# Kernel tuning notes

Measured on AMD Instinct MI355X. Metric: run time of the kernel, lower is better.

## Reference

```python
import jax, jax.numpy as jnp
import numpy as np

B, S, H, E, K = 4, 2048, 2048, 8, 2


def setup_inputs() -> dict:
    key = jax.random.key(0)
    k1, k2, k3 = jax.random.split(key, 3)
    scale = 1.0 / np.sqrt(H)
    return {
        "x": jax.random.normal(k1, (B, S, H), dtype=jnp.float32),
        "Wg": jax.random.normal(k2, (H, E), dtype=jnp.float32) * scale,
        "bg": jnp.zeros((E,), dtype=jnp.float32),
        "W": jax.random.normal(k3, (E, H, H), dtype=jnp.float32) * scale,
        "b": jnp.zeros((E, H), dtype=jnp.float32),
        "topk": K,
    }


def reference(x, Wg, bg, W, b, topk):
    Bsz, Sl, Hd = x.shape
    n_exp = W.shape[0]
    hs = x.reshape(-1, Hd)                              # [T, H] flattened tokens
    # Router: linear gate -> softmax -> top-k -> renormalize
    router_logits = hs @ Wg + bg                        # [T, E]
    probs = jax.nn.softmax(router_logits, axis=-1)
    top_w, sel = jax.lax.top_k(probs, topk)             # [T, K]
    top_w = top_w / jnp.sum(top_w, axis=-1, keepdims=True)
    # Per-token combine coefficient for each expert (sums weights over top-k slots)
    coef = jnp.einsum("tk,tke->te", top_w,
                      jax.nn.one_hot(sel, n_exp, dtype=hs.dtype))  # [T, E]
    # Dense grouped expert MLP: y_e = hs @ W_e + b_e, then weighted combine.
    h = jnp.einsum("th,ehf->etf", hs, W) + b[:, None, :]  # [E, T, H]
    out = jnp.einsum("te,etf->tf", coef, h)               # [T, H]
    return out.reshape(Bsz, Sl, Hd), router_logits
```

## Files before the change

### kernel.cpp

```cpp
#include <hip/hip_runtime.h>
#include <math.h>

#define T_TOK 8192
#define HD    2048
#define NE    8
#define BM    128
#define BN    128
#define NT    (HD / 64)
#define MAXT  136
#define RMAX  17408

typedef __bf16 bf16x4 __attribute__((ext_vector_type(4)));
typedef __bf16 bf16x8 __attribute__((ext_vector_type(8)));
typedef float  f32x4  __attribute__((ext_vector_type(4)));

#define GLOAD16(src, dst)                                                              \
    __builtin_amdgcn_global_load_lds((__attribute__((address_space(1))) void*)(src),   \
                                     (__attribute__((address_space(3))) void*)(dst),   \
                                     16, 0, 0)

__global__ __launch_bounds__(256) void router_cvt_kernel(
    const float* __restrict__ x, const float* __restrict__ Wg,
    const float* __restrict__ bg, float* __restrict__ logits_out,
    int* __restrict__ tok_exp, float* __restrict__ tok_w,
    __bf16* __restrict__ xb)
{
    const int lane = threadIdx.x & 63;
    const int wv   = threadIdx.x >> 6;
    const int t    = blockIdx.x * 4 + wv;
    const float* xr  = x  + (size_t)t * HD;
    __bf16*      xbr = xb + (size_t)t * HD;

    float acc[8] = {0.f,0.f,0.f,0.f,0.f,0.f,0.f,0.f};
#pragma unroll
    for (int j = 0; j < 8; ++j) {
        const int h0 = j * 256 + lane * 4;
        float4 xv = *reinterpret_cast<const float4*>(xr + h0);
        bf16x4 bv;
        bv[0] = (__bf16)xv.x; bv[1] = (__bf16)xv.y;
        bv[2] = (__bf16)xv.z; bv[3] = (__bf16)xv.w;
        *reinterpret_cast<bf16x4*>(xbr + h0) = bv;

        const float4* wg = reinterpret_cast<const float4*>(Wg + (size_t)h0 * NE);
        float xs[4] = {xv.x, xv.y, xv.z, xv.w};
#pragma unroll
        for (int r = 0; r < 4; ++r) {
            float4 wa = wg[r * 2], wb = wg[r * 2 + 1];
            acc[0] += xs[r] * wa.x; acc[1] += xs[r] * wa.y;
            acc[2] += xs[r] * wa.z; acc[3] += xs[r] * wa.w;
            acc[4] += xs[r] * wb.x; acc[5] += xs[r] * wb.y;
            acc[6] += xs[r] * wb.z; acc[7] += xs[r] * wb.w;
        }
    }
#pragma unroll
    for (int off = 32; off; off >>= 1) {
#pragma unroll
        for (int e = 0; e < 8; ++e) acc[e] += __shfl_xor(acc[e], off);
    }
    if (lane == 0) {
        float lg[8];
#pragma unroll
        for (int e = 0; e < 8; ++e) lg[e] = acc[e] + bg[e];
        float4* lo = reinterpret_cast<float4*>(logits_out + (size_t)t * NE);
        lo[0] = make_float4(lg[0], lg[1], lg[2], lg[3]);
        lo[1] = make_float4(lg[4], lg[5], lg[6], lg[7]);
        int i0 = 0;
        for (int e = 1; e < 8; ++e) if (lg[e] > lg[i0]) i0 = e;
        int i1 = (i0 == 0) ? 1 : 0;
        for (int e = 0; e < 8; ++e) if (e != i0 && lg[e] > lg[i1]) i1 = e;
        float d = expf(lg[i1] - lg[i0]);
        float inv = 1.0f / (1.0f + d);
        tok_exp[t * 2]     = i0;
        tok_exp[t * 2 + 1] = i1;
        tok_w[t * 2]       = inv;
        tok_w[t * 2 + 1]   = d * inv;
    }
}

__global__ __launch_bounds__(256) void hist_kernel(const int* __restrict__ tok_exp,
                                                   int* __restrict__ cnt)
{
    __shared__ int h[NE];
    if (threadIdx.x < NE) h[threadIdx.x] = 0;
    __syncthreads();
    int s = blockIdx.x * 256 + threadIdx.x;
    atomicAdd(&h[tok_exp[s]], 1);
    __syncthreads();
    if (threadIdx.x < NE) atomicAdd(&cnt[threadIdx.x], h[threadIdx.x]);
}

__global__ __launch_bounds__(256) void wt_kernel(const float* __restrict__ W,
                                                 __bf16* __restrict__ Wt)
{
    const int e  = blockIdx.z;
    const int k0 = blockIdx.y * 64;
    const int f0 = blockIdx.x * 64;
    __shared__ float T[64][65];

    const int t  = threadIdx.x;
    const int fi = (t & 15) * 4;
    const int kb = t >> 4;
    const float* src = W + (size_t)e * HD * HD + (size_t)(k0 + kb) * HD + f0 + fi;
#pragma unroll
    for (int j = 0; j < 4; ++j) {
        float4 v = *reinterpret_cast<const float4*>(src + (size_t)j * 16 * HD);
        int k = kb + j * 16;
        T[k][fi + 0] = v.x;
        T[k][fi + 1] = v.y;
        T[k][fi + 2] = v.z;
        T[k][fi + 3] = v.w;
    }
    __syncthreads();
    const int f  = t >> 2;
    const int kc = (t & 3) * 16;
    bf16x8 o0, o1;
#pragma unroll
    for (int j = 0; j < 8; ++j) o0[j] = (__bf16)T[kc + j][f];
#pragma unroll
    for (int j = 0; j < 8; ++j) o1[j] = (__bf16)T[kc + 8 + j][f];
    __bf16* dst = Wt + (size_t)e * HD * HD + (size_t)(f0 + f) * HD + k0 + kc;
    *reinterpret_cast<bf16x8*>(dst)     = o0;
    *reinterpret_cast<bf16x8*>(dst + 8) = o1;
}

__global__ void scan_kernel(const int* __restrict__ cnt, int* __restrict__ cursor,
                            int* __restrict__ tile_exp, int* __restrict__ tile_row0,
                            int* __restrict__ ntiles)
{
    if (threadIdx.x == 0) {
        int off = 0, nt = 0;
        for (int e = 0; e < NE; ++e) {
            cursor[e] = off;
            int c = cnt[e];
            int tiles = (c + 127) >> 7;
            for (int i = 0; i < tiles; ++i) {
                tile_exp[nt]  = e;
                tile_row0[nt] = off + (i << 7);
                ++nt;
            }
            off += tiles << 7;
        }
        *ntiles = nt;
    }
}

__global__ __launch_bounds__(256) void scatter_kernel(
    const int* __restrict__ tok_exp, const float* __restrict__ tok_w,
    int* __restrict__ cursor, int* __restrict__ row_token, float* __restrict__ row_coef)
{
    __shared__ int lcnt[NE];
    __shared__ int lbase[NE];
    const int tid = threadIdx.x;
    if (tid < NE) lcnt[tid] = 0;
    __syncthreads();
    const int s = blockIdx.x * 256 + tid;
    const int e = tok_exp[s];
    const int r = atomicAdd(&lcnt[e], 1);
    __syncthreads();
    if (tid < NE) lbase[tid] = atomicAdd(&cursor[tid], lcnt[tid]);
    __syncthreads();
    const int pos = lbase[e] + r;
    row_token[pos] = s >> 1;
    row_coef[pos]  = tok_w[s];
}

__global__ __launch_bounds__(256, 2) void moe_gemm_128(
    const __bf16* __restrict__ xb, const __bf16* __restrict__ Wt,
    const float* __restrict__ bexp,
    const int* __restrict__ tile_exp, const int* __restrict__ tile_row0,
    const int* __restrict__ ntiles_p, const int* __restrict__ row_token,
    const float* __restrict__ row_coef, float* __restrict__ out)
{
    const int rt = blockIdx.y;
    if (rt >= *ntiles_p) return;
    const int e  = tile_exp[rt];
    const int r0 = tile_row0[rt];
    const int cb = blockIdx.x * BN;

    __shared__ __align__(16) char lds[65536];

    const int tid  = threadIdx.x;
    const int lane = tid & 63;
    const int wv   = tid >> 6;
    const int wr   = (wv >> 1) * 64;
    const int wc   = (wv & 1) * 64;

    const int colS = ((((tid & 7) * 16) ^ (((tid >> 3) & 7) << 4))) >> 1;

    const __bf16* srcA[4];
    const __bf16* srcB[4];
#pragma unroll
    for (int i = 0; i < 4; ++i) {
        int gr  = i * 32 + (tid >> 3);
        int tok = row_token[r0 + gr];
        if (tok < 0) tok = 0;
        srcA[i] = xb + (size_t)tok * HD + colS;
        srcB[i] = Wt + ((size_t)e << 22) + (size_t)(cb + gr) * HD + colS;
    }

    f32x4 acc[4][4];
#pragma unroll
    for (int m = 0; m < 4; ++m)
#pragma unroll
        for (int n = 0; n < 4; ++n) acc[m][n] = (f32x4){0.f, 0.f, 0.f, 0.f};

    const int fr    = lane & 15;
    const int swz   = (lane & 7) << 4;
    const int koff0 = (((lane >> 4) * 16)      ) ^ swz;
    const int koff1 = (((lane >> 4) * 16) + 64 ) ^ swz;

    {
        char* d0 = lds + wv * 1024;
        char* d1 = d0 + 32768;
#pragma unroll
        for (int i = 0; i < 4; ++i) GLOAD16(srcA[i], d0 + i * 4096);
#pragma unroll
        for (int i = 0; i < 4; ++i) GLOAD16(srcB[i], d0 + 16384 + i * 4096);
#pragma unroll
        for (int i = 0; i < 4; ++i) GLOAD16(srcA[i] + 64, d1 + i * 4096);
#pragma unroll
        for (int i = 0; i < 4; ++i) GLOAD16(srcB[i] + 64, d1 + 16384 + i * 4096);
    }

#pragma unroll 2
    for (int t = 0; t < NT; ++t) {
        if (t < NT - 1) { asm volatile("s_waitcnt vmcnt(8)" ::: "memory"); }
        else            { asm volatile("s_waitcnt vmcnt(0)" ::: "memory"); }
        __builtin_amdgcn_s_barrier();

        const char* ab = lds + (t & 1) * 32768;
        const char* bb = ab + 16384;

        bf16x8 bfr0[4], bfr1[4];
#pragma unroll
        for (int n = 0; n < 4; ++n) {
            int rowb = (wc + n * 16 + fr) << 7;
            bfr0[n] = *reinterpret_cast<const bf16x8*>(bb + (rowb + koff0));
            bfr1[n] = *reinterpret_cast<const bf16x8*>(bb + (rowb + koff1));
        }
        __builtin_amdgcn_s_setprio(1);
#pragma unroll
        for (int m = 0; m < 4; ++m) {
            int rowa = (wr + m * 16 + fr) << 7;
            bf16x8 a0 = *reinterpret_cast<const bf16x8*>(ab + (rowa + koff0));
            bf16x8 a1 = *reinterpret_cast<const bf16x8*>(ab + (rowa + koff1));
#pragma unroll
            for (int n = 0; n < 4; ++n) {
                acc[m][n] = __builtin_amdgcn_mfma_f32_16x16x32_bf16(a0, bfr0[n], acc[m][n], 0, 0, 0);
                acc[m][n] = __builtin_amdgcn_mfma_f32_16x16x32_bf16(a1, bfr1[n], acc[m][n], 0, 0, 0);
            }
        }
        __builtin_amdgcn_s_setprio(0);

        if (t < NT - 2) {
            asm volatile("s_waitcnt lgkmcnt(0)" ::: "memory");
            __builtin_amdgcn_s_barrier();
            const int nk = (t + 2) * 64;
            char* dA = lds + (t & 1) * 32768 + wv * 1024;
#pragma unroll
            for (int i = 0; i < 4; ++i) GLOAD16(srcA[i] + nk, dA + i * 4096);
#pragma unroll
            for (int i = 0; i < 4; ++i) GLOAD16(srcB[i] + nk, dA + 16384 + i * 4096);
        }
    }

    const int rj = (lane >> 4) * 4;
    float bias_[4];
#pragma unroll
    for (int n = 0; n < 4; ++n)
        bias_[n] = bexp[(size_t)e * HD + cb + wc + n * 16 + fr];

#pragma unroll
    for (int m = 0; m < 4; ++m) {
        const int lr = wr + m * 16 + rj;
        int tok[4]; float cf[4];
#pragma unroll
        for (int j = 0; j < 4; ++j) {
            tok[j] = row_token[r0 + lr + j];
            cf[j]  = row_coef[r0 + lr + j];
        }
#pragma unroll
        for (int n = 0; n < 4; ++n) {
            const int f = cb + wc + n * 16 + fr;
#pragma unroll
            for (int j = 0; j < 4; ++j) {
                if (tok[j] >= 0)
                    atomicAdd(&out[(size_t)tok[j] * HD + f], (acc[m][n][j] + bias_[n]) * cf[j]);
            }
        }
    }
}

extern "C" void kernel_launch(void* const* d_in, const int* in_sizes, int n_in,
                              void* d_out, int out_size, void* d_ws, size_t ws_size,
                              hipStream_t stream)
{
    (void)in_sizes; (void)n_in; (void)out_size; (void)ws_size;

    const float* x  = (const float*)d_in[0];
    const float* Wg = (const float*)d_in[1];
    const float* bg = (const float*)d_in[2];
    const float* W  = (const float*)d_in[3];
    const float* b  = (const float*)d_in[4];

    float* out    = (float*)d_out;
    float* logits = out + (size_t)T_TOK * HD;

    char* p = (char*)d_ws;
    int*   cnt       = (int*)p;   p += NE * 4;
    int*   cursor    = (int*)p;   p += NE * 4;
    int*   ntiles    = (int*)p;   p += 8;
    int*   tile_exp  = (int*)p;   p += MAXT * 4;
    int*   tile_row0 = (int*)p;   p += MAXT * 4;
    int*   tok_exp   = (int*)p;   p += T_TOK * 2 * 4;
    float* tok_w     = (float*)p; p += T_TOK * 2 * 4;
    int*   row_token = (int*)p;   p += RMAX * 4;
    float* row_coef  = (float*)p; p += RMAX * 4;
    p = (char*)(((size_t)p + 255) & ~(size_t)255);
    __bf16* xb = (__bf16*)p;      p += (size_t)T_TOK * HD * 2;
    __bf16* Wt = (__bf16*)p;      p += (size_t)NE * HD * HD * 2;

    hipMemsetAsync(cnt, 0, NE * 4, stream);
    hipMemsetAsync(row_token, 0xFF, RMAX * 4, stream);
    hipMemsetAsync(out, 0, (size_t)T_TOK * HD * sizeof(float), stream);

    router_cvt_kernel<<<T_TOK / 4, 256, 0, stream>>>(x, Wg, bg, logits,
                                                     tok_exp, tok_w, xb);
    wt_kernel<<<dim3(HD / 64, HD / 64, NE), 256, 0, stream>>>(W, Wt);
    hist_kernel<<<T_TOK * 2 / 256, 256, 0, stream>>>(tok_exp, cnt);
    scan_kernel<<<1, 64, 0, stream>>>(cnt, cursor, tile_exp, tile_row0, ntiles);
    scatter_kernel<<<T_TOK * 2 / 256, 256, 0, stream>>>(tok_exp, tok_w, cursor,
                                                        row_token, row_coef);

    dim3 grid(HD / BN, MAXT);
    moe_gemm_128<<<grid, 256, 0, stream>>>(xb, Wt, b, tile_exp, tile_row0, ntiles,
                                           row_token, row_coef, out);
}
```

Measured before the change: 334.0 us.

## Load expert weight fragments straight into registers instead of staging through LDS

The B operand (expert weights) is now fetched from global memory directly into a double-buffered register array in MFMA fragment layout, instead of going through LDS with global_load_lds. Only the A tile is staged in LDS, so the LDS footprint halves and the launch bound is raised to 3 blocks per CU to use the freed space. The goal is to cut LDS traffic and ds_read latency and to raise occupancy. The cost is about 64 extra VGPRs for the fragments, which risks spills under the tighter register cap. B reads become less coalesced and are duplicated across waves that share columns, and compiler-inserted waits on the register loads may break the hand-tuned vmcnt pipelining.

```diff
diff --git a/kernel.cpp b/kernel.cpp
--- a/kernel.cpp
+++ b/kernel.cpp
@@ -18,6 +18,8 @@
     __builtin_amdgcn_global_load_lds((__attribute__((address_space(1))) void*)(src),   \
                                      (__attribute__((address_space(3))) void*)(dst),   \
                                      16, 0, 0)
+
+#define MEMFENCE() asm volatile("" ::: "memory")
 
 __global__ __launch_bounds__(256) void router_cvt_kernel(
     const float* __restrict__ x, const float* __restrict__ Wg,
@@ -164,7 +166,7 @@
     row_coef[pos]  = tok_w[s];
 }
 
-__global__ __launch_bounds__(256, 2) void moe_gemm_128(
+__global__ __launch_bounds__(256, 3) void moe_gemm_128(
     const __bf16* __restrict__ xb, const __bf16* __restrict__ Wt,
     const float* __restrict__ bexp,
     const int* __restrict__ tile_exp, const int* __restrict__ tile_row0,
@@ -177,7 +179,7 @@
     const int r0 = tile_row0[rt];
     const int cb = blockIdx.x * BN;
 
-    __shared__ __align__(16) char lds[65536];
+    __shared__ __align__(16) char lds[32768];
 
     const int tid  = threadIdx.x;
     const int lane = tid & 63;
@@ -188,15 +190,17 @@
     const int colS = ((((tid & 7) * 16) ^ (((tid >> 3) & 7) << 4))) >> 1;
 
     const __bf16* srcA[4];
-    const __bf16* srcB[4];
 #pragma unroll
     for (int i = 0; i < 4; ++i) {
         int gr  = i * 32 + (tid >> 3);
         int tok = row_token[r0 + gr];
         if (tok < 0) tok = 0;
         srcA[i] = xb + (size_t)tok * HD + colS;
-        srcB[i] = Wt + ((size_t)e << 22) + (size_t)(cb + gr) * HD + colS;
-    }
+    }
+
+    const int fr = lane & 15;
+    const int fk = (lane >> 4) * 8;
+    const __bf16* bbase = Wt + ((size_t)e << 22) + (size_t)(cb + wc + fr) * HD + fk;
 
     f32x4 acc[4][4];
 #pragma unroll
@@ -204,40 +208,41 @@
 #pragma unroll
         for (int n = 0; n < 4; ++n) acc[m][n] = (f32x4){0.f, 0.f, 0.f, 0.f};
 
-    const int fr    = lane & 15;
     const int swz   = (lane & 7) << 4;
     const int koff0 = (((lane >> 4) * 16)      ) ^ swz;
     const int koff1 = (((lane >> 4) * 16) + 64 ) ^ swz;
 
+    bf16x8 breg[2][4][2];
+
     {
         char* d0 = lds + wv * 1024;
-        char* d1 = d0 + 32768;
+        char* d1 = d0 + 16384;
 #pragma unroll
         for (int i = 0; i < 4; ++i) GLOAD16(srcA[i], d0 + i * 4096);
 #pragma unroll
-        for (int i = 0; i < 4; ++i) GLOAD16(srcB[i], d0 + 16384 + i * 4096);
+        for (int n = 0; n < 4; ++n)
+#pragma unroll
+            for (int ks = 0; ks < 2; ++ks)
+                breg[0][n][ks] = *reinterpret_cast<const bf16x8*>(bbase + n * 16 * HD + ks * 32);
+        MEMFENCE();
 #pragma unroll
         for (int i = 0; i < 4; ++i) GLOAD16(srcA[i] + 64, d1 + i * 4096);
 #pragma unroll
-        for (int i = 0; i < 4; ++i) GLOAD16(srcB[i] + 64, d1 + 16384 + i * 4096);
+        for (int n = 0; n < 4; ++n)
+#pragma unroll
+            for (int ks = 0; ks < 2; ++ks)
+                breg[1][n][ks] = *reinterpret_cast<const bf16x8*>(bbase + n * 16 * HD + 64 + ks * 32);
+        MEMFENCE();
     }
 
 #pragma unroll 2
     for (int t = 0; t < NT; ++t) {
-        if (t < NT - 1) { asm volatile("s_waitcnt vmcnt(8)" ::: "memory"); }
+        if (t < NT - 1) { asm volatile("s_waitcnt vmcnt(12)" ::: "memory"); }
         else            { asm volatile("s_waitcnt vmcnt(0)" ::: "memory"); }
         __builtin_amdgcn_s_barrier();
 
-        const char* ab = lds + (t & 1) * 32768;
-        const char* bb = ab + 16384;
-
-        bf16x8 bfr0[4], bfr1[4];
-#pragma unroll
-        for (int n = 0; n < 4; ++n) {
-            int rowb = (wc + n * 16 + fr) << 7;
-            bfr0[n] = *reinterpret_cast<const bf16x8*>(bb + (rowb + koff0));
-            bfr1[n] = *reinterpret_cast<const bf16x8*>(bb + (rowb + koff1));
-        }
+        const char* ab = lds + (t & 1) * 16384;
+
         __builtin_amdgcn_s_setprio(1);
 #pragma unroll
         for (int m = 0; m < 4; ++m) {
@@ -246,8 +251,8 @@
             bf16x8 a1 = *reinterpret_cast<const bf16x8*>(ab + (rowa + koff1));
 #pragma unroll
             for (int n = 0; n < 4; ++n) {
-                acc[m][n] = __builtin_amdgcn_mfma_f32_16x16x32_bf16(a0, bfr0[n], acc[m][n], 0, 0, 0);
-                acc[m][n] = __builtin_amdgcn_mfma_f32_16x16x32_bf16(a1, bfr1[n], acc[m][n], 0, 0, 0);
+                acc[m][n] = __builtin_amdgcn_mfma_f32_16x16x32_bf16(a0, breg[t & 1][n][0], acc[m][n], 0, 0, 0);
+                acc[m][n] = __builtin_amdgcn_mfma_f32_16x16x32_bf16(a1, breg[t & 1][n][1], acc[m][n], 0, 0, 0);
             }
         }
         __builtin_amdgcn_s_setprio(0);
@@ -255,12 +260,17 @@
         if (t < NT - 2) {
             asm volatile("s_waitcnt lgkmcnt(0)" ::: "memory");
             __builtin_amdgcn_s_barrier();
+            MEMFENCE();
             const int nk = (t + 2) * 64;
-            char* dA = lds + (t & 1) * 32768 + wv * 1024;
+            char* dA = lds + (t & 1) * 16384 + wv * 1024;
 #pragma unroll
             for (int i = 0; i < 4; ++i) GLOAD16(srcA[i] + nk, dA + i * 4096);
 #pragma unroll
-            for (int i = 0; i < 4; ++i) GLOAD16(srcB[i] + nk, dA + 16384 + i * 4096);
+            for (int n = 0; n < 4; ++n)
+#pragma unroll
+                for (int ks = 0; ks < 2; ++ks)
+                    breg[t & 1][n][ks] = *reinterpret_cast<const bf16x8*>(bbase + n * 16 * HD + nk + ks * 32);
+            MEMFENCE();
         }
     }
 
```

Measured after the change: 485.5 us. 1.45x slower.
